# Kernel tuning notes

Measured on AMD Instinct MI355X. Metric: run time of the kernel, lower is better.

The kernel has to match this reference:

```python
import jax, jax.numpy as jnp
import numpy as np

EPS = 1e-3  # keras LayerNormalization default epsilon


def _layernorm(y, gamma, beta):
    m = jnp.mean(y, axis=-1, keepdims=True)
    v = jnp.var(y, axis=-1, keepdims=True)
    return (y - m) * jax.lax.rsqrt(v + EPS) * gamma + beta


def setup_inputs() -> dict:
    key = jax.random.key(0)
    ks = jax.random.split(key, 3)
    B, S, D, F = 4, 8192, 512, 2048
    x = jax.random.normal(ks[0], (B, S, D), dtype=jnp.float32)
    W1 = jax.random.normal(ks[1], (D, F), dtype=jnp.float32) * (1.0 / np.sqrt(D))
    b1 = jnp.zeros((F,), dtype=jnp.float32)
    W2 = jax.random.normal(ks[2], (F, D), dtype=jnp.float32) * (1.0 / np.sqrt(F))
    b2 = jnp.zeros((D,), dtype=jnp.float32)
    g1 = jnp.ones((D,), dtype=jnp.float32)
    be1 = jnp.zeros((D,), dtype=jnp.float32)
    g2 = jnp.ones((D,), dtype=jnp.float32)
    be2 = jnp.zeros((D,), dtype=jnp.float32)
    return {"x": x, "W1": W1, "b1": b1, "W2": W2, "b2": b2,
            "g1": g1, "be1": be1, "g2": g2, "be2": be2}


def reference(x, W1, b1, W2, b2, g1, be1, g2, be2):
    # 2D FFT over (seq, embed) axes; keep real part (FNet mixing)
    fft = jnp.real(jnp.fft.fft2(x.astype(jnp.complex64), axes=(-2, -1)))
    proj_input = _layernorm(x + fft, g1, be1)
    # FFN: Dense(dense_dim, relu) -> Dense(embed_dim)
    h = jax.nn.relu(jnp.einsum('bsd,df->bsf', proj_input, W1) + b1)
    proj_output = jnp.einsum('bsf,fd->bsd', h, W2) + b2
    return _layernorm(proj_input + proj_output, g2, be2)
```

## Files before the change

kernel.cpp:

```cpp
#include <hip/hip_runtime.h>

typedef unsigned short u16;
typedef unsigned int u32;
typedef short short8 __attribute__((ext_vector_type(8)));
typedef float f32x4 __attribute__((ext_vector_type(4)));

#define LN_EPS 1e-3f
#define PI2 6.28318530717958647692f
#define AS1 __attribute__((address_space(1)))
#define AS3 __attribute__((address_space(3)))

__device__ __forceinline__ u16 f2bf(float f) {
  u32 u = __float_as_uint(f);
  u += 0x7fffu + ((u >> 16) & 1u);
  return (u16)(u >> 16);
}
__device__ __forceinline__ float bf2f(u16 h) {
  return __uint_as_float(((u32)h) << 16);
}

__global__ __launch_bounds__(256) void prep_w(const float* __restrict__ W,
                                              u16* __restrict__ Wt, int R, int C) {
  __shared__ float tile[32][33];
  const int ct = C >> 5;
  int bc = blockIdx.x % ct;
  int br = blockIdx.x / ct;
  int tx = threadIdx.x & 31, ty = threadIdx.x >> 5;
  int r0 = br << 5, c0 = bc << 5;
#pragma unroll
  for (int i = 0; i < 32; i += 8)
    tile[ty + i][tx] = W[(size_t)(r0 + ty + i) * C + c0 + tx];
  __syncthreads();
#pragma unroll
  for (int i = 0; i < 32; i += 8)
    Wt[(size_t)(c0 + ty + i) * R + r0 + tx] = f2bf(tile[tx][ty + i]);
}

__global__ __launch_bounds__(256) void transpose_x(const float* __restrict__ x,
                                                   float* __restrict__ xt) {
  __shared__ float tile[32][33];
  int blk = blockIdx.x;
  int b = blk >> 12;
  int rem = blk & 4095;
  int st = rem >> 4;
  int dt = rem & 15;
  int tx = threadIdx.x & 31, ty = threadIdx.x >> 5;
  int s0 = st << 5, d0 = dt << 5;
#pragma unroll
  for (int i = 0; i < 32; i += 8)
    tile[ty + i][tx] = x[(((size_t)(b << 13) + s0 + ty + i) << 9) + d0 + tx];
  __syncthreads();
#pragma unroll
  for (int i = 0; i < 32; i += 8)
    xt[(((size_t)(b << 9) + d0 + ty + i) << 13) + s0 + tx] = tile[tx][ty + i];
}

__device__ __constant__ float C16r[8] = {1.f, 0.92387953f, 0.70710678f, 0.38268343f,
                                         0.f, -0.38268343f, -0.70710678f, -0.92387953f};
__device__ __constant__ float C16i[8] = {0.f, -0.38268343f, -0.70710678f, -0.92387953f,
                                         -1.f, -0.92387953f, -0.70710678f, -0.38268343f};
__device__ __constant__ float C8r[4] = {1.f, 0.70710678f, 0.f, -0.70710678f};
__device__ __constant__ float C8i[4] = {0.f, -0.70710678f, -1.f, -0.70710678f};
__device__ __constant__ float C4r[2] = {1.f, 0.f};
__device__ __constant__ float C4i[2] = {0.f, -1.f};
__device__ __constant__ float C32r[16] = {
    1.f, 0.98078528f, 0.92387953f, 0.83146961f, 0.70710678f, 0.55557023f,
    0.38268343f, 0.19509032f, 0.f, -0.19509032f, -0.38268343f, -0.55557023f,
    -0.70710678f, -0.83146961f, -0.92387953f, -0.98078528f};
__device__ __constant__ float C32i[16] = {
    0.f, -0.19509032f, -0.38268343f, -0.55557023f, -0.70710678f, -0.83146961f,
    -0.92387953f, -0.98078528f, -1.f, -0.98078528f, -0.92387953f, -0.83146961f,
    -0.70710678f, -0.55557023f, -0.38268343f, -0.19509032f};
__device__ __constant__ int REV4[16] = {0, 8, 4, 12, 2, 10, 6, 14,
                                        1, 9, 5, 13, 3, 11, 7, 15};

__device__ __forceinline__ constexpr int rev4c(int v) {
  return ((v & 1) << 3) | ((v & 2) << 1) | ((v & 4) >> 1) | ((v & 8) >> 3);
}

#define BFLY(ar, ai, br, bi, wr, wi)                 \
  {                                                  \
    float dr_ = (ar) - (br), di_ = (ai) - (bi);      \
    (ar) += (br);                                    \
    (ai) += (bi);                                    \
    (br) = dr_ * (wr)-di_ * (wi);                    \
    (bi) = dr_ * (wi) + di_ * (wr);                  \
  }

__global__ __launch_bounds__(512) void fft_s(float* __restrict__ X, float* __restrict__ Xim) {
  __shared__ float zr[8448], zi[8448];
  const int t = threadIdx.x;
  const int b = blockIdx.x >> 8;
  const int d0 = (blockIdx.x & 255) << 1;
  float* r0 = X + (((size_t)(b << 9) + d0) << 13);
  float* r1 = r0 + 8192;

  float xr[16], xi[16];
#pragma unroll
  for (int e = 0; e < 16; ++e) {
    xr[e] = r0[t + (e << 9)];
    xi[e] = r1[t + (e << 9)];
  }

  float c1, s1;
  sincosf(-PI2 * (float)t * (1.0f / 8192.0f), &s1, &c1);
  float c2 = c1 * c1 - s1 * s1, s2 = 2.f * c1 * s1;
  float c4 = c2 * c2 - s2 * s2, s4 = 2.f * c2 * s2;
  float c8 = c4 * c4 - s4 * s4, s8 = 2.f * c4 * s4;
#pragma unroll
  for (int e = 0; e < 8; ++e) {
    float wr = c1 * C16r[e] - s1 * C16i[e];
    float wi = c1 * C16i[e] + s1 * C16r[e];
    BFLY(xr[e], xi[e], xr[e + 8], xi[e + 8], wr, wi);
  }
#pragma unroll
  for (int e = 0; e < 16; ++e) {
    if ((e & 4) == 0) {
      int eb = e & 3;
      float wr = c2 * C8r[eb] - s2 * C8i[eb];
      float wi = c2 * C8i[eb] + s2 * C8r[eb];
      BFLY(xr[e], xi[e], xr[e + 4], xi[e + 4], wr, wi);
    }
  }
#pragma unroll
  for (int e = 0; e < 16; ++e) {
    if (((e >> 1) & 1) == 0) {
      int eb = e & 1;
      float wr = c4 * C4r[eb] - s4 * C4i[eb];
      float wi = c4 * C4i[eb] + s4 * C4r[eb];
      BFLY(xr[e], xi[e], xr[e + 2], xi[e + 2], wr, wi);
    }
  }
#pragma unroll
  for (int e = 0; e < 16; e += 2) {
    BFLY(xr[e], xi[e], xr[e + 1], xi[e + 1], c8, s8);
  }

#pragma unroll
  for (int e = 0; e < 16; ++e) {
    int idx = t + (e << 9);
    int a = idx + (idx >> 5);
    zr[a] = xr[e];
    zi[a] = xi[e];
  }
  __syncthreads();
  {
    const int f = t >> 5, l = t & 31;
#pragma unroll
    for (int e = 0; e < 16; ++e) {
      int idx = (f << 9) + (e << 5) + l;
      int a = idx + (idx >> 5);
      xr[e] = zr[a];
      xi[e] = zi[a];
    }
    float bc1, bs1;
    sincosf(-PI2 * (float)l * (1.0f / 512.0f), &bs1, &bc1);
    float bc2 = bc1 * bc1 - bs1 * bs1, bs2 = 2.f * bc1 * bs1;
    float bc4 = bc2 * bc2 - bs2 * bs2, bs4 = 2.f * bc2 * bs2;
    float bc8 = bc4 * bc4 - bs4 * bs4, bs8 = 2.f * bc4 * bs4;
#pragma unroll
    for (int e = 0; e < 8; ++e) {
      float wr = bc1 * C16r[e] - bs1 * C16i[e];
      float wi = bc1 * C16i[e] + bs1 * C16r[e];
      BFLY(xr[e], xi[e], xr[e + 8], xi[e + 8], wr, wi);
    }
#pragma unroll
    for (int e = 0; e < 16; ++e) {
      if (((e >> 2) & 1) == 0) {
        int eb = e & 3;
        float wr = bc2 * C8r[eb] - bs2 * C8i[eb];
        float wi = bc2 * C8i[eb] + bs2 * C8r[eb];
        BFLY(xr[e], xi[e], xr[e + 4], xi[e + 4], wr, wi);
      }
    }
#pragma unroll
    for (int e = 0; e < 16; ++e) {
      if (((e >> 1) & 1) == 0) {
        int eb = e & 1;
        float wr = bc4 * C4r[eb] - bs4 * C4i[eb];
        float wi = bc4 * C4i[eb] + bs4 * C4r[eb];
        BFLY(xr[e], xi[e], xr[e + 2], xi[e + 2], wr, wi);
      }
    }
#pragma unroll
    for (int e = 0; e < 16; e += 2) {
      BFLY(xr[e], xi[e], xr[e + 1], xi[e + 1], bc8, bs8);
    }
    __syncthreads();
#pragma unroll
    for (int e = 0; e < 16; ++e) {
      int idx = (f << 9) + (e << 5) + l;
      int a = idx + (idx >> 5);
      zr[a] = xr[e];
      zi[a] = xi[e];
    }
  }
  __syncthreads();
#pragma unroll
  for (int j = 0; j < 16; ++j) {
    int idx = (t << 4) + j;
    int a = idx + (idx >> 5);
    xr[j] = zr[a];
    xi[j] = zi[a];
  }

  {
    const int odd = t & 1;
#pragma unroll
    for (int j = 0; j < 16; ++j) {
      float pr = __shfl_xor(xr[j], 1);
      float pi = __shfl_xor(xi[j], 1);
      if (!odd) {
        xr[j] += pr;
        xi[j] += pi;
      } else {
        float dr = pr - xr[j], di = pi - xi[j];
        xr[j] = dr * C32r[j] - di * C32i[j];
        xi[j] = dr * C32i[j] + di * C32r[j];
      }
    }
#pragma unroll
    for (int j = 0; j < 8; ++j) {
      BFLY(xr[j], xi[j], xr[j + 8], xi[j + 8], C16r[j], C16i[j]);
    }
#pragma unroll
    for (int j = 0; j < 16; ++j) {
      if (((j >> 2) & 1) == 0) {
        BFLY(xr[j], xi[j], xr[j + 4], xi[j + 4], C8r[j & 3], C8i[j & 3]);
      }
    }
#pragma unroll
    for (int j = 0; j < 16; ++j) {
      if (((j >> 1) & 1) == 0) {
        BFLY(xr[j], xi[j], xr[j + 2], xi[j + 2], C4r[j & 1], C4i[j & 1]);
      }
    }
#pragma unroll
    for (int j = 0; j < 16; j += 2) {
      BFLY(xr[j], xi[j], xr[j + 1], xi[j + 1], 1.0f, 0.0f);
    }
  }

  __syncthreads();
  {
    const int rt = __brev((u32)t) >> 23;
#pragma unroll
    for (int j = 0; j < 16; ++j) {
      int k = (REV4[j] << 9) | rt;
      int a = k + (k >> 5);
      zr[a] = xr[j];
      zi[a] = xi[j];
    }
  }
  __syncthreads();

  float* i0 = Xim + (((size_t)(b << 9) + d0) << 13);
  float* i1 = i0 + 8192;
#pragma unroll
  for (int e = 0; e < 16; ++e) {
    int k = t + (e << 9);
    int nk = (8192 - k) & 8191;
    int ka = k + (k >> 5), na = nk + (nk >> 5);
    float zrk = zr[ka], zik = zi[ka], zrn = zr[na], zin = zi[na];
    r0[k] = 0.5f * (zrk + zrn);
    i0[k] = 0.5f * (zik - zin);
    r1[k] = 0.5f * (zik + zin);
    i1[k] = 0.5f * (zrn - zrk);
  }
}

__global__ __launch_bounds__(256) void fft_d_ln(
    const float* __restrict__ Xre, const float* __restrict__ Xim,
    const float* __restrict__ x, const float* __restrict__ g1,
    const float* __restrict__ be1, u16* __restrict__ proj) {
  __shared__ float buf[16 * 528];
  const int tid = threadIdx.x;
  const int b = blockIdx.x >> 9;
  const int s0 = (blockIdx.x & 511) << 4;
  const int row = tid >> 4, t = tid & 15;
  const int so = tid & 15, dd = tid >> 4;

  float xr[32], xi[32];

#pragma unroll
  for (int it = 0; it < 32; ++it) {
    int d = dd + (it << 4);
    buf[so * 516 + d] = Xre[(((size_t)(b << 9) + d) << 13) + s0 + so];
  }
  __syncthreads();
#pragma unroll
  for (int e = 0; e < 32; ++e) xr[e] = buf[row * 516 + t + (e << 4)];
  __syncthreads();
#pragma unroll
  for (int it = 0; it < 32; ++it) {
    int d = dd + (it << 4);
    buf[so * 516 + d] = Xim[(((size_t)(b << 9) + d) << 13) + s0 + so];
  }
  __syncthreads();
#pragma unroll
  for (int e = 0; e < 32; ++e) xi[e] = buf[row * 516 + t + (e << 4)];
  __syncthreads();

  float c1, s1;
  sincosf(-PI2 * (float)t * (1.0f / 512.0f), &s1, &c1);
  float c2 = c1 * c1 - s1 * s1, s2 = 2.f * c1 * s1;
  float c4 = c2 * c2 - s2 * s2, s4 = 2.f * c2 * s2;
  float c8 = c4 * c4 - s4 * s4, s8 = 2.f * c4 * s4;
  float c16 = c8 * c8 - s8 * s8, s16 = 2.f * c8 * s8;
#pragma unroll
  for (int e = 0; e < 16; ++e) {
    float wr = c1 * C32r[e] - s1 * C32i[e];
    float wi = c1 * C32i[e] + s1 * C32r[e];
    BFLY(xr[e], xi[e], xr[e + 16], xi[e + 16], wr, wi);
  }
#pragma unroll
  for (int e = 0; e < 32; ++e) {
    if ((e & 8) == 0) {
      int eb = e & 7;
      float wr = c2 * C16r[eb] - s2 * C16i[eb];
      float wi = c2 * C16i[eb] + s2 * C16r[eb];
      BFLY(xr[e], xi[e], xr[e + 8], xi[e + 8], wr, wi);
    }
  }
#pragma unroll
  for (int e = 0; e < 32; ++e) {
    if ((e & 4) == 0) {
      int eb = e & 3;
      float wr = c4 * C8r[eb] - s4 * C8i[eb];
      float wi = c4 * C8i[eb] + s4 * C8r[eb];
      BFLY(xr[e], xi[e], xr[e + 4], xi[e + 4], wr, wi);
    }
  }
#pragma unroll
  for (int e = 0; e < 32; ++e) {
    if ((e & 2) == 0) {
      int eb = e & 1;
      float wr = c8 * C4r[eb] - s8 * C4i[eb];
      float wi = c8 * C4i[eb] + s8 * C4r[eb];
      BFLY(xr[e], xi[e], xr[e + 2], xi[e + 2], wr, wi);
    }
  }
#pragma unroll
  for (int e = 0; e < 32; e += 2) {
    BFLY(xr[e], xi[e], xr[e + 1], xi[e + 1], c16, s16);
  }

#pragma unroll
  for (int e = 0; e < 32; ++e) {
    int p = (e << 4) + t;
    buf[row * 528 + p + (p >> 5)] = xr[e];
  }
  __syncthreads();
#pragma unroll
  for (int j = 0; j < 32; ++j) xr[j] = buf[row * 528 + 33 * t + j];
  __syncthreads();
#pragma unroll
  for (int e = 0; e < 32; ++e) {
    int p = (e << 4) + t;
    buf[row * 528 + p + (p >> 5)] = xi[e];
  }
  __syncthreads();
#pragma unroll
  for (int j = 0; j < 32; ++j) xi[j] = buf[row * 528 + 33 * t + j];
  __syncthreads();

#pragma unroll
  for (int o = 0; o < 32; o += 16) {
#pragma unroll
    for (int j = 0; j < 8; ++j)
      BFLY(xr[o + j], xi[o + j], xr[o + j + 8], xi[o + j + 8], C16r[j], C16i[j]);
#pragma unroll
    for (int j = 0; j < 16; ++j)
      if ((j & 4) == 0)
        BFLY(xr[o + j], xi[o + j], xr[o + j + 4], xi[o + j + 4], C8r[j & 3], C8i[j & 3]);
#pragma unroll
    for (int j = 0; j < 16; ++j)
      if ((j & 2) == 0)
        BFLY(xr[o + j], xi[o + j], xr[o + j + 2], xi[o + j + 2], C4r[j & 1], C4i[j & 1]);
#pragma unroll
    for (int j = 0; j < 16; j += 2)
      BFLY(xr[o + j], xi[o + j], xr[o + j + 1], xi[o + j + 1], 1.0f, 0.0f);
  }

  {
    const int rt4 = __brev((u32)t) >> 28;
#pragma unroll
    for (int j = 0; j < 16; ++j) {
      const int rj = rev4c(j);
      buf[row * 528 + 33 * rj + rt4] = xr[j];
      buf[row * 528 + 33 * rj + 16 + rt4] = xr[16 + j];
    }
  }
  __syncthreads();

  const int s = s0 + row;
  const float* xrow = x + (((size_t)(b << 13) + s) << 9);
  float v[32];
  float sum = 0.f, sum2 = 0.f;
#pragma unroll
  for (int m = 0; m < 32; ++m) {
    int d = t + (m << 4);
    float val = buf[row * 528 + d + (d >> 5)] + xrow[d];
    v[m] = val;
    sum += val;
    sum2 += val * val;
  }
#pragma unroll
  for (int m = 1; m < 16; m <<= 1) {
    sum += __shfl_xor(sum, m, 16);
    sum2 += __shfl_xor(sum2, m, 16);
  }
  float mean = sum * (1.0f / 512.0f);
  float var = sum2 * (1.0f / 512.0f) - mean * mean;
  float scl = 1.0f / sqrtf(var + LN_EPS);
  u16* prow = proj + (((size_t)(b << 13) + s) << 9);
#pragma unroll
  for (int m = 0; m < 32; ++m) {
    int d = t + (m << 4);
    prow[d] = f2bf((v[m] - mean) * scl * g1[d] + be1[d]);
  }
}

template <bool RELU, bool OUT_BF16, int GH>
__global__ __launch_bounds__(256, 2) void gemm_bt(
    const u16* __restrict__ A, const u16* __restrict__ Bt,
    const float* __restrict__ bias, void* __restrict__ Cout,
    int M, int N, int K) {
  const int tid = threadIdx.x;
  const int lane = tid & 63;
  const int wave = tid >> 6;
  const int wm = wave >> 1, wn = wave & 1;
  const int llo = lane & 15, lhi = lane >> 4;

  const int nwg = gridDim.x;
  const int q = nwg >> 3;
  const int b2 = ((int)blockIdx.x & 7) * q + ((int)blockIdx.x >> 3);
  const int NT = N >> 7;
  const int GSZ = GH * NT;
  const int grp = b2 / GSZ;
  const int r = b2 - grp * GSZ;
  const int tn = r / GH;
  const int tm = grp * GH + (r - tn * GH);
  const int m0 = tm << 7, n0 = tn << 7;

  __shared__ short8 smem[2048];
  char* ldsA = (char*)&smem[0];
  char* ldsB = ldsA + 16384;

  f32x4 acc[4][4] = {};

  const int trow = tid >> 3;
  const int ksw = (((tid & 7) ^ (trow & 7)) << 3);
  const int wbase = wave << 10;
  const int swz = (llo & 7) << 4;

  const int KT = K >> 6;
  for (int kt = 0; kt < KT; ++kt) {
    const int k0 = (kt << 6) + ksw;
    __syncthreads();
#pragma unroll
    for (int r4 = 0; r4 < 4; ++r4) {
      const int grow = (r4 << 5) + trow;
      const u16* ga = A + (size_t)(m0 + grow) * K + k0;
      const u16* gb = Bt + (size_t)(n0 + grow) * K + k0;
      __builtin_amdgcn_global_load_lds((const AS1 void*)ga,
                                       (AS3 void*)(ldsA + (r4 << 12) + wbase), 16, 0, 0);
      __builtin_amdgcn_global_load_lds((const AS1 void*)gb,
                                       (AS3 void*)(ldsB + (r4 << 12) + wbase), 16, 0, 0);
    }
    __syncthreads();
#pragma unroll
    for (int kk = 0; kk < 2; ++kk) {
      const int cbx = ((kk << 6) | (lhi << 4)) ^ swz;
      short8 af[4], bfr[4];
#pragma unroll
      for (int mt = 0; mt < 4; ++mt)
        af[mt] = *(const short8*)(ldsA + (((wm << 6) + (mt << 4) + llo) << 7) + cbx);
#pragma unroll
      for (int nt = 0; nt < 4; ++nt)
        bfr[nt] = *(const short8*)(ldsB + (((wn << 6) + (nt << 4) + llo) << 7) + cbx);
#pragma unroll
      for (int mt = 0; mt < 4; ++mt)
#pragma unroll
        for (int nt = 0; nt < 4; ++nt)
          acc[mt][nt] =
              __builtin_amdgcn_mfma_f32_16x16x32_bf16(af[mt], bfr[nt], acc[mt][nt], 0, 0, 0);
    }
  }
#pragma unroll
  for (int nt = 0; nt < 4; ++nt) {
    const int col = n0 + (wn << 6) + (nt << 4) + llo;
    const float bv = bias[col];
#pragma unroll
    for (int mt = 0; mt < 4; ++mt) {
      const int rbase = m0 + (wm << 6) + (mt << 4) + (lhi << 2);
#pragma unroll
      for (int j = 0; j < 4; ++j) {
        float v = acc[mt][nt][j] + bv;
        if (RELU) v = fmaxf(v, 0.0f);
        if (OUT_BF16) ((u16*)Cout)[(size_t)(rbase + j) * N + col] = f2bf(v);
        else          ((float*)Cout)[(size_t)(rbase + j) * N + col] = v;
      }
    }
  }
}

template <bool RELU, bool OUT_BF16, int GH>
__global__ __launch_bounds__(512, 2) void gemm256(
    const u16* __restrict__ A, const u16* __restrict__ Bt,
    const float* __restrict__ bias, void* __restrict__ Cout,
    int M, int N, int K) {
  const int tid = threadIdx.x;
  const int lane = tid & 63;
  const int wave = tid >> 6;
  const int wm = wave >> 2;
  const int wn = wave & 3;
  const int llo = lane & 15, lhi = lane >> 4;

  const int nwg = gridDim.x;
  const int q = nwg >> 3;
  const int b2 = ((int)blockIdx.x & 7) * q + ((int)blockIdx.x >> 3);
  const int NT = N >> 8;
  const int GSZ = GH * NT;
  const int grp = b2 / GSZ;
  const int rr = b2 - grp * GSZ;
  const int tn = rr / GH;
  const int tm = grp * GH + (rr - tn * GH);
  const int m0 = tm << 8, n0 = tn << 8;

  __shared__ short8 smem[8192];
  char* ldsA = (char*)&smem[0];
  char* ldsB = ldsA + 65536;

  f32x4 acc[8][4] = {};

  const int trow = tid >> 3;
  const int ksw = ((tid & 7) ^ (trow & 7)) << 3;
  const int swz = (llo & 7) << 4;
  const int cb0 = (lhi << 4) ^ swz;
  const char* Ab0 = ldsA + wm * 16384 + llo * 128;
  const char* Bb0 = ldsB + (wn >> 1) * 16384 + (((wn & 1) << 6) + llo) * 128;

#define GLDS(g_, d_) __builtin_amdgcn_global_load_lds((const AS1 void*)(g_), (AS3 void*)(d_), 16, 0, 0)
#define STAGE_A(kt, hf) {                                                        \
    const u16* g_ = A + (size_t)(m0 + ((hf) << 7) + trow) * K + ((kt) << 6) + ksw; \
    char* d_ = ldsA + (((kt)&1) << 15) + ((hf) << 14) + tid * 16;                \
    GLDS(g_, d_); GLDS(g_ + ((size_t)64) * K, d_ + 8192); }
#define STAGE_B(kt, hf) {                                                        \
    const u16* g_ = Bt + (size_t)(n0 + ((hf) << 7) + trow) * K + ((kt) << 6) + ksw; \
    char* d_ = ldsB + (((kt)&1) << 15) + ((hf) << 14) + tid * 16;                \
    GLDS(g_, d_); GLDS(g_ + ((size_t)64) * K, d_ + 8192); }
#define BAR() { __builtin_amdgcn_sched_barrier(0); __builtin_amdgcn_s_barrier(); \
                __builtin_amdgcn_sched_barrier(0); }
#define VMW(n_) { asm volatile("s_waitcnt vmcnt(" #n_ ")" ::: "memory"); }

  const int KT = K >> 6;
  STAGE_A(0, 0); STAGE_A(0, 1); STAGE_B(0, 0); STAGE_B(0, 1);
  STAGE_B(1, 0); STAGE_B(1, 1);
  VMW(0);
  BAR();

  for (int t0 = 0; t0 < KT; t0 += 2) {
    const bool pf = (t0 + 2 < KT);
#pragma unroll
    for (int s = 0; s < 2; ++s) {
      const char* Abase = Ab0 + (s << 15);
      const char* Bbase = Bb0 + (s << 15);
      short8 bfr[4][2];
      {
#pragma unroll
        for (int fn = 0; fn < 4; ++fn) {
          bfr[fn][0] = *(const short8*)(Bbase + fn * 2048 + cb0);
          bfr[fn][1] = *(const short8*)(Bbase + fn * 2048 + (cb0 ^ 64));
        }
        short8 af[2][2];
#pragma unroll
        for (int i = 0; i < 2; ++i) {
          af[i][0] = *(const short8*)(Abase + i * 2048 + cb0);
          af[i][1] = *(const short8*)(Abase + i * 2048 + (cb0 ^ 64));
        }
        if (s == 0) {
          STAGE_A(t0 + 1, 0); STAGE_A(t0 + 1, 1);
        } else if (pf) {
          STAGE_A(t0 + 2, 0); STAGE_A(t0 + 2, 1);
        }
        BAR();
        __builtin_amdgcn_s_setprio(1);
#pragma unroll
        for (int i = 0; i < 2; ++i)
#pragma unroll
          for (int fn = 0; fn < 4; ++fn)
#pragma unroll
            for (int kk = 0; kk < 2; ++kk)
              acc[i][fn] = __builtin_amdgcn_mfma_f32_16x16x32_bf16(
                  af[i][kk], bfr[fn][kk], acc[i][fn], 0, 0, 0);
        __builtin_amdgcn_s_setprio(0);
        BAR();
      }
#pragma unroll
      for (int qq = 1; qq < 4; ++qq) {
        short8 af[2][2];
#pragma unroll
        for (int i = 0; i < 2; ++i) {
          af[i][0] = *(const short8*)(Abase + (qq * 2 + i) * 2048 + cb0);
          af[i][1] = *(const short8*)(Abase + (qq * 2 + i) * 2048 + (cb0 ^ 64));
        }
        if (pf) {
          if (s == 0) {
            if (qq == 1) STAGE_B(t0 + 2, 0);
            if (qq == 2) STAGE_B(t0 + 2, 1);
          } else {
            if (qq == 1) STAGE_B(t0 + 3, 0);
            if (qq == 2) STAGE_B(t0 + 3, 1);
          }
        }
        BAR();
        __builtin_amdgcn_s_setprio(1);
#pragma unroll
        for (int i = 0; i < 2; ++i)
#pragma unroll
          for (int fn = 0; fn < 4; ++fn)
#pragma unroll
            for (int kk = 0; kk < 2; ++kk)
              acc[qq * 2 + i][fn] = __builtin_amdgcn_mfma_f32_16x16x32_bf16(
                  af[i][kk], bfr[fn][kk], acc[qq * 2 + i][fn], 0, 0, 0);
        __builtin_amdgcn_s_setprio(0);
        if (qq == 3) VMW(4);
        BAR();
      }
    }
  }
#undef GLDS
#undef STAGE_A
#undef STAGE_B
#undef BAR
#undef VMW

  float bv[4];
#pragma unroll
  for (int fn = 0; fn < 4; ++fn) bv[fn] = bias[n0 + (wn << 6) + (fn << 4) + llo];
#pragma unroll
  for (int fm = 0; fm < 8; ++fm) {
#pragma unroll
    for (int j = 0; j < 4; ++j) {
      const size_t row = (size_t)(m0 + (wm << 7) + (fm << 4) + (lhi << 2) + j);
#pragma unroll
      for (int fn = 0; fn < 4; ++fn) {
        const int col = n0 + (wn << 6) + (fn << 4) + llo;
        float v = acc[fm][fn][j] + bv[fn];
        if (RELU) v = fmaxf(v, 0.0f);
        if (OUT_BF16) ((u16*)Cout)[row * N + col] = f2bf(v);
        else          ((float*)Cout)[row * N + col] = v;
      }
    }
  }
}

__global__ __launch_bounds__(256) void ln2_kernel(
    float* __restrict__ out, const u16* __restrict__ proj,
    const float* __restrict__ g2, const float* __restrict__ be2) {
  const int lane = threadIdx.x & 63;
  const int row = blockIdx.x * 4 + (threadIdx.x >> 6);
  float* orow = out + ((size_t)row << 9);
  const u16* prow = proj + ((size_t)row << 9);
  const int d0 = lane << 3;
  f32x4 a0 = *(const f32x4*)(orow + d0);
  f32x4 a1 = *(const f32x4*)(orow + d0 + 4);
  short8 p = *(const short8*)(prow + d0);
  float y[8];
  float sum = 0.f, sum2 = 0.f;
#pragma unroll
  for (int m = 0; m < 8; ++m) {
    float v = (m < 4 ? a0[m] : a1[m - 4]) + bf2f((u16)p[m]);
    y[m] = v; sum += v; sum2 += v * v;
  }
#pragma unroll
  for (int m = 1; m < 64; m <<= 1) {
    sum += __shfl_xor(sum, m, 64);
    sum2 += __shfl_xor(sum2, m, 64);
  }
  float mean = sum * (1.0f / 512.0f);
  float var = sum2 * (1.0f / 512.0f) - mean * mean;
  float scl = 1.0f / sqrtf(var + LN_EPS);
  f32x4 g0 = *(const f32x4*)(g2 + d0);
  f32x4 g1v = *(const f32x4*)(g2 + d0 + 4);
  f32x4 e0 = *(const f32x4*)(be2 + d0);
  f32x4 e1 = *(const f32x4*)(be2 + d0 + 4);
  f32x4 o0, o1;
#pragma unroll
  for (int m = 0; m < 4; ++m) o0[m] = (y[m] - mean) * scl * g0[m] + e0[m];
#pragma unroll
  for (int m = 0; m < 4; ++m) o1[m] = (y[m + 4] - mean) * scl * g1v[m] + e1[m];
  *(f32x4*)(orow + d0) = o0;
  *(f32x4*)(orow + d0 + 4) = o1;
}

extern "C" void kernel_launch(void* const* d_in, const int* in_sizes, int n_in,
                              void* d_out, int out_size, void* d_ws, size_t ws_size,
                              hipStream_t stream) {
  const float* x   = (const float*)d_in[0];
  const float* W1  = (const float*)d_in[1];
  const float* b1  = (const float*)d_in[2];
  const float* W2  = (const float*)d_in[3];
  const float* b2  = (const float*)d_in[4];
  const float* g1  = (const float*)d_in[5];
  const float* be1 = (const float*)d_in[6];
  const float* g2  = (const float*)d_in[7];
  const float* be2 = (const float*)d_in[8];

  char* ws = (char*)d_ws;
  float* xre  = (float*)(ws);
  float* xim  = (float*)(ws + (64u << 20));
  u16*   proj = (u16*)(ws + (128u << 20));
  u16*   w1t  = (u16*)(ws + (160u << 20));
  u16*   w2t  = (u16*)(ws + (162u << 20));
  u16*   h    = (u16*)(ws);

  prep_w<<<1024, 256, 0, stream>>>(W1, w1t, 512, 2048);
  prep_w<<<1024, 256, 0, stream>>>(W2, w2t, 2048, 512);
  transpose_x<<<16384, 256, 0, stream>>>(x, xre);
  fft_s<<<1024, 512, 0, stream>>>(xre, xim);
  fft_d_ln<<<2048, 256, 0, stream>>>(xre, xim, x, g1, be1, proj);
  gemm_bt<true, true, 8><<<4096, 256, 0, stream>>>(proj, w1t, b1, (void*)h, 32768, 2048, 512);
  gemm256<false, false, 2><<<256, 512, 0, stream>>>(h, w2t, b2, d_out, 32768, 512, 2048);
  ln2_kernel<<<8192, 256, 0, stream>>>((float*)d_out, proj, g2, be2);
  (void)in_sizes; (void)n_in; (void)out_size; (void)ws_size;
}
```

Measured before the change: 316.6 us.

## Exploit Hermitian symmetry of real-input FFT to halve seq-axis spectrum work

Because the input is real, the 2D spectrum satisfies X[S-k, D-d] = conj(X[k,d]), so only seq frequencies 0..4096 need computing along the embed axis. fft_s now writes only half the spectrum (plus the Nyquist bin), and fft_d_ln processes 257 tiles per batch, emitting the real part for both row k and its mirror 8192-k with the embed index reflected. This roughly halves the spectrum writes and embed-axis FFT work, but each block now does two layer norms and the last tile per batch is partly idle.

```diff
diff --git a/kernel.cpp b/kernel.cpp
--- a/kernel.cpp
+++ b/kernel.cpp
@@ -257,7 +257,7 @@
   float* i0 = Xim + (((size_t)(b << 9) + d0) << 13);
   float* i1 = i0 + 8192;
 #pragma unroll
-  for (int e = 0; e < 16; ++e) {
+  for (int e = 0; e < 8; ++e) {
     int k = t + (e << 9);
     int nk = (8192 - k) & 8191;
     int ka = k + (k >> 5), na = nk + (nk >> 5);
@@ -267,6 +267,14 @@
     r1[k] = 0.5f * (zik + zin);
     i1[k] = 0.5f * (zrn - zrk);
   }
+  if (t == 0) {
+    const int ka = 4096 + (4096 >> 5);
+    float zrk = zr[ka], zik = zi[ka];
+    r0[4096] = zrk;
+    i0[4096] = 0.f;
+    r1[4096] = zik;
+    i1[4096] = 0.f;
+  }
 }
 
 __global__ __launch_bounds__(256) void fft_d_ln(
@@ -275,8 +283,9 @@
     const float* __restrict__ be1, u16* __restrict__ proj) {
   __shared__ float buf[16 * 528];
   const int tid = threadIdx.x;
-  const int b = blockIdx.x >> 9;
-  const int s0 = (blockIdx.x & 511) << 4;
+  const int b = blockIdx.x / 257;
+  const int kt = blockIdx.x - b * 257;
+  const int s0 = kt << 4;
   const int row = tid >> 4, t = tid & 15;
   const int so = tid & 15, dd = tid >> 4;
 
@@ -393,31 +402,64 @@
   }
   __syncthreads();
 
-  const int s = s0 + row;
-  const float* xrow = x + (((size_t)(b << 13) + s) << 9);
-  float v[32];
-  float sum = 0.f, sum2 = 0.f;
-#pragma unroll
-  for (int m = 0; m < 32; ++m) {
-    int d = t + (m << 4);
-    float val = buf[row * 528 + d + (d >> 5)] + xrow[d];
-    v[m] = val;
-    sum += val;
-    sum2 += val * val;
-  }
-#pragma unroll
-  for (int m = 1; m < 16; m <<= 1) {
-    sum += __shfl_xor(sum, m, 16);
-    sum2 += __shfl_xor(sum2, m, 16);
-  }
-  float mean = sum * (1.0f / 512.0f);
-  float var = sum2 * (1.0f / 512.0f) - mean * mean;
-  float scl = 1.0f / sqrtf(var + LN_EPS);
-  u16* prow = proj + (((size_t)(b << 13) + s) << 9);
-#pragma unroll
-  for (int m = 0; m < 32; ++m) {
-    int d = t + (m << 4);
-    prow[d] = f2bf((v[m] - mean) * scl * g1[d] + be1[d]);
+  const int k = s0 + row;
+  {
+    const float* xrow = x + (((size_t)(b << 13) + k) << 9);
+    float v[32];
+    float sum = 0.f, sum2 = 0.f;
+#pragma unroll
+    for (int m = 0; m < 32; ++m) {
+      int d = t + (m << 4);
+      float val = buf[row * 528 + d + (d >> 5)] + xrow[d];
+      v[m] = val;
+      sum += val;
+      sum2 += val * val;
+    }
+#pragma unroll
+    for (int m = 1; m < 16; m <<= 1) {
+      sum += __shfl_xor(sum, m, 16);
+      sum2 += __shfl_xor(sum2, m, 16);
+    }
+    float mean = sum * (1.0f / 512.0f);
+    float var = sum2 * (1.0f / 512.0f) - mean * mean;
+    float scl = 1.0f / sqrtf(var + LN_EPS);
+    if (k <= 4096) {
+      u16* prow = proj + (((size_t)(b << 13) + k) << 9);
+#pragma unroll
+      for (int m = 0; m < 32; ++m) {
+        int d = t + (m << 4);
+        prow[d] = f2bf((v[m] - mean) * scl * g1[d] + be1[d]);
+      }
+    }
+  }
+  if (k >= 1 && k <= 4095) {
+    const int sm = 8192 - k;
+    const float* xrow = x + (((size_t)(b << 13) + sm) << 9);
+    float v[32];
+    float sum = 0.f, sum2 = 0.f;
+#pragma unroll
+    for (int m = 0; m < 32; ++m) {
+      int d = t + (m << 4);
+      int dm = (512 - d) & 511;
+      float val = buf[row * 528 + dm + (dm >> 5)] + xrow[d];
+      v[m] = val;
+      sum += val;
+      sum2 += val * val;
+    }
+#pragma unroll
+    for (int m = 1; m < 16; m <<= 1) {
+      sum += __shfl_xor(sum, m, 16);
+      sum2 += __shfl_xor(sum2, m, 16);
+    }
+    float mean = sum * (1.0f / 512.0f);
+    float var = sum2 * (1.0f / 512.0f) - mean * mean;
+    float scl = 1.0f / sqrtf(var + LN_EPS);
+    u16* prow = proj + (((size_t)(b << 13) + sm) << 9);
+#pragma unroll
+    for (int m = 0; m < 32; ++m) {
+      int d = t + (m << 4);
+      prow[d] = f2bf((v[m] - mean) * scl * g1[d] + be1[d]);
+    }
   }
 }
 
@@ -720,7 +762,7 @@
   prep_w<<<1024, 256, 0, stream>>>(W2, w2t, 2048, 512);
   transpose_x<<<16384, 256, 0, stream>>>(x, xre);
   fft_s<<<1024, 512, 0, stream>>>(xre, xim);
-  fft_d_ln<<<2048, 256, 0, stream>>>(xre, xim, x, g1, be1, proj);
+  fft_d_ln<<<1028, 256, 0, stream>>>(xre, xim, x, g1, be1, proj);
   gemm_bt<true, true, 8><<<4096, 256, 0, stream>>>(proj, w1t, b1, (void*)h, 32768, 2048, 512);
   gemm256<false, false, 2><<<256, 512, 0, stream>>>(h, w2t, b2, d_out, 32768, 512, 2048);
   ln2_kernel<<<8192, 256, 0, stream>>>((float*)d_out, proj, g2, be2);
```

New measurement: 280.2 us. 11.5% less time.
